# Kernel tuning notes

Hardware: AMD Instinct MI355X
Metric: run time of the kernel (lower is better)

## Reference

```python
import jax, jax.numpy as jnp
import numpy as np

N_NODES = 50000
N_EDGES = 1600000
IN_CH = 128
HEADS = 4
HEAD_DIM = 32  # out_channels // heads = 128 // 4
NEG_SLOPE = 0.2


def setup_inputs() -> dict:
    key = jax.random.key(0)
    ks = jax.random.split(key, 6)
    x = jax.random.normal(ks[0], (N_NODES, IN_CH), dtype=jnp.float32)
    edge_index = jax.random.randint(ks[1], (2, N_EDGES), 0, N_NODES, dtype=jnp.int64)
    W = jax.random.normal(ks[2], (IN_CH, HEADS * HEAD_DIM), dtype=jnp.float32) * 0.1
    att_src = jax.random.normal(ks[3], (HEADS, HEAD_DIM), dtype=jnp.float32) * 0.1
    att_dst = jax.random.normal(ks[4], (HEADS, HEAD_DIM), dtype=jnp.float32) * 0.1
    bias = jax.random.normal(ks[5], (HEADS * HEAD_DIM,), dtype=jnp.float32) * 0.1
    return {"x": x, "edge_index": edge_index, "W": W,
            "att_src": att_src, "att_dst": att_dst, "bias": bias}


def reference(x, edge_index, W, att_src, att_dst, bias):
    N = x.shape[0]
    # linear projection, split heads: [N, H, C]
    h = (x @ W).reshape(N, HEADS, HEAD_DIM)
    # per-node attention logits: [N, H]
    a_src = jnp.einsum('nhc,hc->nh', h, att_src)
    a_dst = jnp.einsum('nhc,hc->nh', h, att_dst)
    # add self loops (PyG default)
    loops = jnp.arange(N, dtype=edge_index.dtype)
    src = jnp.concatenate([edge_index[0], loops])  # message source j
    dst = jnp.concatenate([edge_index[1], loops])  # message target i
    # edge attention scores: [E_total, H]
    alpha = jax.nn.leaky_relu(a_src[src] + a_dst[dst], NEG_SLOPE)
    # segment softmax over incoming edges per destination node
    amax = jax.ops.segment_max(alpha, dst, num_segments=N)
    alpha = jnp.exp(alpha - amax[dst])
    denom = jax.ops.segment_sum(alpha, dst, num_segments=N)
    alpha = alpha / (denom[dst] + 1e-16)
    # weighted scatter-aggregate: [N, H, C]
    msg = h[src] * alpha[:, :, None]
    out = jax.ops.segment_sum(msg, dst, num_segments=N)
    out = out.reshape(N, HEADS * HEAD_DIM) + bias
    return jax.nn.elu(out)
```

## Files before the change

kernel.cpp:

```cpp
#include <hip/hip_runtime.h>

typedef unsigned short u16;
typedef unsigned int u32;

#define CH 128
#define NHEAD 4
#define NEG_SLOPE 0.2f
#define ROWS_PER_BLOCK 32
#define XPAD 132

#define LOG_NPB 7
#define NPB 128
#define NBMAX 400
#define BCAP 6144
#define KMB 6
#define GPAD 16
#define BINA_BLOCKS 256

typedef __attribute__((ext_vector_type(8))) short bf16x8;
typedef __attribute__((ext_vector_type(4))) float f32x4;

static __device__ __forceinline__ float bitf(u32 i) {
    float f; __builtin_memcpy(&f, &i, 4); return f;
}
static __device__ __forceinline__ float bflo(u32 v) { return bitf(v << 16); }
static __device__ __forceinline__ float bfhi(u32 v) { return bitf(v & 0xffff0000u); }
static __device__ __forceinline__ u16 f2bf(float f) {
    u32 i; __builtin_memcpy(&i, &f, 4);
    return (u16)((i + 0x7fffu + ((i >> 16) & 1u)) >> 16);
}
static __device__ __forceinline__ float lrelu(float v) { return v > 0.f ? v : NEG_SLOPE * v; }

static __device__ __forceinline__ int ei_at(const int* __restrict__ ei, int mode32, size_t idx) {
    return mode32 ? ei[idx] : ei[2 * idx];
}

__global__ __launch_bounds__(256) void init_kernel(
    const float* __restrict__ W, uint4* __restrict__ Wsw, int* __restrict__ gcur, int nGcur)
{
    const int t = blockIdx.x * 256 + threadIdx.x;
    if (t < 2048) {
        const int lane = t & 63, ks = (t >> 6) & 3, nt = t >> 8;
        const int col = nt * 16 + (lane & 15);
        const int kb = ks * 32 + ((lane >> 4) << 2);
        u16 v[8];
#pragma unroll
        for (int j = 0; j < 8; ++j) {
            int kk = kb + (j & 3) + ((j >> 2) << 4);
            v[j] = f2bf(W[(size_t)kk * CH + col]);
        }
        uint4 q;
        q.x = (u32)v[0] | ((u32)v[1] << 16);
        q.y = (u32)v[2] | ((u32)v[3] << 16);
        q.z = (u32)v[4] | ((u32)v[5] << 16);
        q.w = (u32)v[6] | ((u32)v[7] << 16);
        Wsw[t] = q;
    }
    for (int i = t; i < nGcur; i += 4096) gcur[i] = 0;
}

__global__ __launch_bounds__(256) void gemmbin_kernel(
    const float* __restrict__ x, const uint4* __restrict__ Wsw,
    const float* __restrict__ att_src, const float* __restrict__ att_dst,
    u16* __restrict__ h, float* __restrict__ asrc, float* __restrict__ adst, int N,
    const int* __restrict__ ei, int* __restrict__ gcur, u32* __restrict__ rec,
    int E, int NB)
{
    __shared__ float xs[ROWS_PER_BLOCK][XPAD];
    __shared__ uint4 Wb[2048];

    const int tid = threadIdx.x;

    if (blockIdx.x < BINA_BLOCKS) {
        int* hist  = (int*)&xs[0][0];
        int* hbase = hist + NBMAX;
        int* hcur  = hbase + NBMAX;
        const int mode32 = __syncthreads_or(ei[2 * tid + 1] != 0);
        for (int b = tid; b < NB; b += 256) { hist[b] = 0; hcur[b] = 0; }
        __syncthreads();
        const int chunk = (E + BINA_BLOCKS - 1) / BINA_BLOCKS;
        const int beg0 = blockIdx.x * chunk;
        const int end0 = min(E, beg0 + chunk);
#pragma unroll 4
        for (int e = beg0 + tid; e < end0; e += 256) {
            int dj = ei_at(ei, mode32, (size_t)E + e);
            atomicAdd(&hist[dj >> LOG_NPB], 1);
        }
        __syncthreads();
        for (int b = tid; b < NB; b += 256) {
            int c = hist[b];
            hbase[b] = c ? atomicAdd(&gcur[b * GPAD], c) : 0;
        }
        __syncthreads();
#pragma unroll 4
        for (int e = beg0 + tid; e < end0; e += 256) {
            int dj = ei_at(ei, mode32, (size_t)E + e);
            int sj = ei_at(ei, mode32, (size_t)e);
            int bkt = dj >> LOG_NPB;
            int r = atomicAdd(&hcur[bkt], 1);
            int pos = hbase[bkt] + r;
            if (pos < BCAP)
                rec[(size_t)bkt * BCAP + pos] = ((u32)sj << LOG_NPB) | (u32)(dj & (NPB - 1));
        }
        return;
    }

    const int gb = blockIdx.x - BINA_BLOCKS;
    const int r0b = gb * ROWS_PER_BLOCK;
#pragma unroll
    for (int i = 0; i < 8; ++i) Wb[tid + i * 256] = Wsw[tid + i * 256];
#pragma unroll
    for (int i = 0; i < 4; ++i) {
        int f = tid + i * 256;
        int row = f >> 5;
        int col = (f & 31) * 4;
        if (r0b + row < N)
            *(float4*)&xs[row][col] = *(const float4*)(x + (size_t)(r0b + row) * CH + col);
    }
    __syncthreads();

    const int lane = tid & 63;
    const int w = tid >> 6;
    const int g = lane >> 4;
    const int a15 = lane & 15;
    const int rt = w & 1;
    const int cb4 = w >> 1;

    f32x4 acc[4] = {};

#pragma unroll
    for (int ks = 0; ks < 4; ++ks) {
        const float* xr = &xs[rt * 16 + a15][ks * 32 + g * 4];
        float4 av0 = *(const float4*)xr;
        float4 av1 = *(const float4*)(xr + 16);
        float av[8] = {av0.x, av0.y, av0.z, av0.w, av1.x, av1.y, av1.z, av1.w};
        bf16x8 ahi, alo;
#pragma unroll
        for (int j = 0; j < 8; ++j) {
            u16 hb = f2bf(av[j]);
            ahi[j] = (short)hb;
            alo[j] = (short)f2bf(av[j] - bflo(hb));
        }
#pragma unroll
        for (int ct = 0; ct < 4; ++ct) {
            bf16x8 b = *(const bf16x8*)&Wb[((cb4 * 4 + ct) * 4 + ks) * 64 + lane];
            acc[ct] = __builtin_amdgcn_mfma_f32_16x16x32_bf16(alo, b, acc[ct], 0, 0, 0);
            acc[ct] = __builtin_amdgcn_mfma_f32_16x16x32_bf16(ahi, b, acc[ct], 0, 0, 0);
        }
    }

    float as_c[4], ad_c[4];
#pragma unroll
    for (int ct = 0; ct < 4; ++ct) {
        int c = cb4 * 64 + ct * 16 + a15;
        as_c[ct] = att_src[c];
        ad_c[ct] = att_dst[c];
    }
#pragma unroll
    for (int i = 0; i < 4; ++i) {
        float s0 = acc[0][i] * as_c[0] + acc[1][i] * as_c[1];
        float s1 = acc[2][i] * as_c[2] + acc[3][i] * as_c[3];
        float d0 = acc[0][i] * ad_c[0] + acc[1][i] * ad_c[1];
        float d1 = acc[2][i] * ad_c[2] + acc[3][i] * ad_c[3];
#pragma unroll
        for (int o = 1; o < 16; o <<= 1) {
            s0 += __shfl_xor(s0, o, 64);
            s1 += __shfl_xor(s1, o, 64);
            d0 += __shfl_xor(d0, o, 64);
            d1 += __shfl_xor(d1, o, 64);
        }
        if (a15 == 0) {
            int row = r0b + rt * 16 + g * 4 + i;
            if (row < N) {
                int hb0 = cb4 * 2;
                asrc[row * NHEAD + hb0]     = s0;
                asrc[row * NHEAD + hb0 + 1] = s1;
                adst[row * NHEAD + hb0]     = d0;
                adst[row * NHEAD + hb0 + 1] = d1;
            }
        }
    }

    __syncthreads();
    u16* ht = (u16*)&xs[0][0];
#pragma unroll
    for (int ct = 0; ct < 4; ++ct)
#pragma unroll
        for (int i = 0; i < 4; ++i)
            ht[(rt * 16 + g * 4 + i) * CH + cb4 * 64 + ct * 16 + a15] = f2bf(acc[ct][i]);
    __syncthreads();
    {
        const u32* ht32 = (const u32*)&xs[0][0];
        const int rw = w * 8;
#pragma unroll
        for (int r = 0; r < 8; ++r) {
            int row = r0b + rw + r;
            if (row < N)
                *(u32*)(h + (size_t)row * CH + lane * 2) = ht32[(rw + r) * 64 + lane];
        }
    }
}

__global__ __launch_bounds__(1024) void binBagg_kernel(
    const u16* __restrict__ h, const float* __restrict__ asrc, const float* __restrict__ adst,
    const int* __restrict__ gcur, const u32* __restrict__ rec,
    const float* __restrict__ bias, float* __restrict__ out, int N)
{
    __shared__ int outb[BCAP + 32];
    __shared__ int lcnt[NPB];
    __shared__ int lsc[NPB];
    __shared__ int lcur[NPB];
    const int tid = threadIdx.x;
    const int bkt = blockIdx.x;
    int cnt0 = gcur[bkt * GPAD];
    cnt0 = cnt0 < BCAP ? cnt0 : BCAP;
    const size_t rbase = (size_t)bkt * BCAP;

    if (tid < NPB) { lcnt[tid] = 0; lcur[tid] = 0; }

    u32 rc[KMB];
#pragma unroll
    for (int k = 0; k < KMB; ++k) {
        int i = tid + k * 1024;
        rc[k] = (i < cnt0) ? rec[rbase + i] : 0xffffffffu;
    }
    __syncthreads();
#pragma unroll
    for (int k = 0; k < KMB; ++k)
        if (rc[k] != 0xffffffffu) atomicAdd(&lcnt[rc[k] & (NPB - 1)], 1);
    __syncthreads();
    if (tid < NPB) lsc[tid] = lcnt[tid];
    __syncthreads();
    for (int o = 1; o < NPB; o <<= 1) {
        int v = (tid < NPB && tid >= o) ? lsc[tid - o] : 0;
        __syncthreads();
        if (tid < NPB) lsc[tid] += v;
        __syncthreads();
    }
#pragma unroll
    for (int k = 0; k < KMB; ++k) {
        if (rc[k] != 0xffffffffu) {
            int local = rc[k] & (NPB - 1);
            int r = atomicAdd(&lcur[local], 1);
            int slot = (lsc[local] - lcnt[local]) + r;
            outb[slot] = (int)(rc[k] >> LOG_NPB);
        }
    }
    __syncthreads();

    const int lane = tid & 63;
    const int wave = tid >> 6;
    const int g = lane >> 4;
    const int l = lane & 15;
    const int c8 = l * 8;
    const int head = l >> 2;

    for (int nl = 0; nl < 8; ++nl) {
        const int local = wave * 8 + nl;
        const int node = (bkt << LOG_NPB) + local;
        if (node >= N) continue;
        const int beg = lsc[local] - lcnt[local];
        const int end = lsc[local];
        const float4 ad4 = *(const float4*)(adst + node * 4);
        const float adh = (head == 0) ? ad4.x : (head == 1) ? ad4.y : (head == 2) ? ad4.z : ad4.w;
        const float4 asl = *(const float4*)(asrc + node * 4);
        const float aslh = (head == 0) ? asl.x : (head == 1) ? asl.y : (head == 2) ? asl.z : asl.w;
        const float mh = lrelu(aslh + adh);

        float acc[8];
#pragma unroll
        for (int k = 0; k < 8; ++k) acc[k] = 0.f;
        float s = 0.f;

        int e = beg + g;
        if (e < end) {
            uint4 hC[4]; float aC[4];
#pragma unroll
            for (int i = 0; i < 4; ++i) {
                int ei = e + 4 * i;
                int j = outb[ei];
                j = ((u32)j < (u32)N) ? j : 0;
                float a = asrc[j * NHEAD + head];
                aC[i] = (ei < end) ? a : -1e30f;
                hC[i] = *(const uint4*)(h + (size_t)j * CH + c8);
            }
            for (;;) {
                const int ebase = e + 16;
                uint4 hP[4]; float aP[4];
#pragma unroll
                for (int i = 0; i < 4; ++i) {
                    int ei = ebase + 4 * i;
                    int j = outb[ei];
                    j = ((u32)j < (u32)N) ? j : 0;
                    float a = asrc[j * NHEAD + head];
                    aP[i] = (ei < end) ? a : -1e30f;
                    hP[i] = *(const uint4*)(h + (size_t)j * CH + c8);
                }
#pragma unroll
                for (int i = 0; i < 4; ++i) {
                    float w = __expf(lrelu(aC[i] + adh) - mh);
                    s += w;
                    acc[0] = fmaf(w, bflo(hC[i].x), acc[0]);
                    acc[1] = fmaf(w, bfhi(hC[i].x), acc[1]);
                    acc[2] = fmaf(w, bflo(hC[i].y), acc[2]);
                    acc[3] = fmaf(w, bfhi(hC[i].y), acc[3]);
                    acc[4] = fmaf(w, bflo(hC[i].z), acc[4]);
                    acc[5] = fmaf(w, bfhi(hC[i].z), acc[5]);
                    acc[6] = fmaf(w, bflo(hC[i].w), acc[6]);
                    acc[7] = fmaf(w, bfhi(hC[i].w), acc[7]);
                }
#pragma unroll
                for (int i = 0; i < 4; ++i) { aC[i] = aP[i]; hC[i] = hP[i]; }
                e = ebase;
                if (e >= end) break;
            }
        }
        if (g == 0) {
            s += 1.0f;
            uint4 hv = *(const uint4*)(h + (size_t)node * CH + c8);
            acc[0] += bflo(hv.x);
            acc[1] += bfhi(hv.x);
            acc[2] += bflo(hv.y);
            acc[3] += bfhi(hv.y);
            acc[4] += bflo(hv.z);
            acc[5] += bfhi(hv.z);
            acc[6] += bflo(hv.w);
            acc[7] += bfhi(hv.w);
        }
#pragma unroll
        for (int o = 16; o < 64; o <<= 1) {
            s += __shfl_xor(s, o, 64);
#pragma unroll
            for (int k = 0; k < 8; ++k) acc[k] += __shfl_xor(acc[k], o, 64);
        }
        if (g == 0) {
            const float inv = 1.f / (s + 1e-16f);
            float o0[8];
#pragma unroll
            for (int k = 0; k < 8; ++k) {
                float v = acc[k] * inv + bias[c8 + k];
                o0[k] = v > 0.f ? v : __expf(v) - 1.f;
            }
            float4 lo = make_float4(o0[0], o0[1], o0[2], o0[3]);
            float4 hi = make_float4(o0[4], o0[5], o0[6], o0[7]);
            *(float4*)(out + (size_t)node * CH + c8) = lo;
            *(float4*)(out + (size_t)node * CH + c8 + 4) = hi;
        }
    }
}

extern "C" void kernel_launch(void* const* d_in, const int* in_sizes, int n_in,
                              void* d_out, int out_size, void* d_ws, size_t ws_size,
                              hipStream_t stream)
{
    const float* x       = (const float*)d_in[0];
    const int*   ei      = (const int*)d_in[1];
    const float* W       = (const float*)d_in[2];
    const float* att_src = (const float*)d_in[3];
    const float* att_dst = (const float*)d_in[4];
    const float* bias    = (const float*)d_in[5];
    float* out = (float*)d_out;
    const int N = in_sizes[0] / CH;
    const int E = in_sizes[1] / 2;
    const int NB = (N + NPB - 1) / NPB;

    char* p = (char*)d_ws;
    auto alloc = [&](size_t bytes) { char* r = p; p += (bytes + 255) & ~(size_t)255; return r; };
    u16*   h    = (u16*)alloc((size_t)N * CH * 2);
    float* asrc = (float*)alloc((size_t)N * NHEAD * 4);
    float* adst = (float*)alloc((size_t)N * NHEAD * 4);
    int*   gcur = (int*)alloc((size_t)NB * GPAD * 4);
    u32*   rec  = (u32*)alloc((size_t)NB * BCAP * 4);
    uint4* Wsw  = (uint4*)alloc((size_t)2048 * 16);

    const int gemmBlocks = (N + ROWS_PER_BLOCK - 1) / ROWS_PER_BLOCK;
    init_kernel<<<16, 256, 0, stream>>>(W, Wsw, gcur, NB * GPAD);
    gemmbin_kernel<<<BINA_BLOCKS + gemmBlocks, 256, 0, stream>>>(
        x, Wsw, att_src, att_dst, h, asrc, adst, N, ei, gcur, rec, E, NB);
    binBagg_kernel<<<NB, 1024, 0, stream>>>(h, asrc, adst, gcur, rec, bias, out, N);
}
```

Measured before the change: 197.3 us.

## Split fused bin-sort/aggregate kernel into CSR build and per-node aggregation kernels

The fused kernel that sorted bucketed edges in shared memory and then aggregated 128 nodes per 1024-thread block is split in two. A 256-thread sort kernel now writes a CSR array plus begin/degree arrays to global memory. A separate aggregation kernel handles one node per wave over N/4 blocks, which should improve load balance and occupancy. The cost is an extra launch and a global round trip for the CSR indices, about 6.4MB written and then read back.

```diff
diff --git a/kernel.cpp b/kernel.cpp
--- a/kernel.cpp
+++ b/kernel.cpp
@@ -13,7 +13,7 @@
 #define NPB 128
 #define NBMAX 400
 #define BCAP 6144
-#define KMB 6
+#define KMAX 24
 #define GPAD 16
 #define BINA_BLOCKS 256
 
@@ -201,12 +201,11 @@
     }
 }
 
-__global__ __launch_bounds__(1024) void binBagg_kernel(
-    const u16* __restrict__ h, const float* __restrict__ asrc, const float* __restrict__ adst,
+__global__ __launch_bounds__(256) void binB_kernel(
     const int* __restrict__ gcur, const u32* __restrict__ rec,
-    const float* __restrict__ bias, float* __restrict__ out, int N)
-{
-    __shared__ int outb[BCAP + 32];
+    int* __restrict__ csr, int* __restrict__ begA, int* __restrict__ degA, int N)
+{
+    __shared__ int outb[BCAP];
     __shared__ int lcnt[NPB];
     __shared__ int lsc[NPB];
     __shared__ int lcur[NPB];
@@ -218,15 +217,15 @@
 
     if (tid < NPB) { lcnt[tid] = 0; lcur[tid] = 0; }
 
-    u32 rc[KMB];
-#pragma unroll
-    for (int k = 0; k < KMB; ++k) {
-        int i = tid + k * 1024;
+    u32 rc[KMAX];
+#pragma unroll
+    for (int k = 0; k < KMAX; ++k) {
+        int i = tid + k * 256;
         rc[k] = (i < cnt0) ? rec[rbase + i] : 0xffffffffu;
     }
     __syncthreads();
 #pragma unroll
-    for (int k = 0; k < KMB; ++k)
+    for (int k = 0; k < KMAX; ++k)
         if (rc[k] != 0xffffffffu) atomicAdd(&lcnt[rc[k] & (NPB - 1)], 1);
     __syncthreads();
     if (tid < NPB) lsc[tid] = lcnt[tid];
@@ -238,7 +237,7 @@
         __syncthreads();
     }
 #pragma unroll
-    for (int k = 0; k < KMB; ++k) {
+    for (int k = 0; k < KMAX; ++k) {
         if (rc[k] != 0xffffffffu) {
             int local = rc[k] & (NPB - 1);
             int r = atomicAdd(&lcur[local], 1);
@@ -247,105 +246,116 @@
         }
     }
     __syncthreads();
-
-    const int lane = tid & 63;
-    const int wave = tid >> 6;
+    for (int i = tid; i < cnt0; i += 256)
+        csr[rbase + i] = outb[i];
+    if (tid < NPB) {
+        int node = (bkt << LOG_NPB) + tid;
+        if (node < N) {
+            begA[node] = (int)rbase + (lsc[tid] - lcnt[tid]);
+            degA[node] = lcnt[tid];
+        }
+    }
+}
+
+__global__ __launch_bounds__(256) void agg_kernel(
+    const u16* __restrict__ h, const float* __restrict__ asrc, const float* __restrict__ adst,
+    const int* __restrict__ begA, const int* __restrict__ degA, const int* __restrict__ csr,
+    const float* __restrict__ bias, float* __restrict__ out, int N)
+{
+    const int lane = threadIdx.x & 63;
+    const int wave = threadIdx.x >> 6;
+    const int node = blockIdx.x * 4 + wave;
+    if (node >= N) return;
     const int g = lane >> 4;
     const int l = lane & 15;
     const int c8 = l * 8;
     const int head = l >> 2;
-
-    for (int nl = 0; nl < 8; ++nl) {
-        const int local = wave * 8 + nl;
-        const int node = (bkt << LOG_NPB) + local;
-        if (node >= N) continue;
-        const int beg = lsc[local] - lcnt[local];
-        const int end = lsc[local];
-        const float4 ad4 = *(const float4*)(adst + node * 4);
-        const float adh = (head == 0) ? ad4.x : (head == 1) ? ad4.y : (head == 2) ? ad4.z : ad4.w;
-        const float4 asl = *(const float4*)(asrc + node * 4);
-        const float aslh = (head == 0) ? asl.x : (head == 1) ? asl.y : (head == 2) ? asl.z : asl.w;
-        const float mh = lrelu(aslh + adh);
-
-        float acc[8];
-#pragma unroll
-        for (int k = 0; k < 8; ++k) acc[k] = 0.f;
-        float s = 0.f;
-
-        int e = beg + g;
-        if (e < end) {
-            uint4 hC[4]; float aC[4];
+    const int beg = begA[node];
+    const int end = beg + degA[node];
+    const float4 ad4 = *(const float4*)(adst + node * 4);
+    const float adh = (head == 0) ? ad4.x : (head == 1) ? ad4.y : (head == 2) ? ad4.z : ad4.w;
+    const float4 asl = *(const float4*)(asrc + node * 4);
+    const float aslh = (head == 0) ? asl.x : (head == 1) ? asl.y : (head == 2) ? asl.z : asl.w;
+    const float mh = lrelu(aslh + adh);
+
+    float acc[8];
+#pragma unroll
+    for (int k = 0; k < 8; ++k) acc[k] = 0.f;
+    float s = 0.f;
+
+    int e = beg + g;
+    if (e < end) {
+        uint4 hC[4]; float aC[4];
+#pragma unroll
+        for (int i = 0; i < 4; ++i) {
+            int ei = e + 4 * i;
+            int j = csr[ei];
+            j = ((u32)j < (u32)N) ? j : 0;
+            float a = asrc[j * NHEAD + head];
+            aC[i] = (ei < end) ? a : -1e30f;
+            hC[i] = *(const uint4*)(h + (size_t)j * CH + c8);
+        }
+        for (;;) {
+            const int ebase = e + 16;
+            uint4 hP[4]; float aP[4];
 #pragma unroll
             for (int i = 0; i < 4; ++i) {
-                int ei = e + 4 * i;
-                int j = outb[ei];
+                int ei = ebase + 4 * i;
+                int j = csr[ei];
                 j = ((u32)j < (u32)N) ? j : 0;
                 float a = asrc[j * NHEAD + head];
-                aC[i] = (ei < end) ? a : -1e30f;
-                hC[i] = *(const uint4*)(h + (size_t)j * CH + c8);
+                aP[i] = (ei < end) ? a : -1e30f;
+                hP[i] = *(const uint4*)(h + (size_t)j * CH + c8);
             }
-            for (;;) {
-                const int ebase = e + 16;
-                uint4 hP[4]; float aP[4];
-#pragma unroll
-                for (int i = 0; i < 4; ++i) {
-                    int ei = ebase + 4 * i;
-                    int j = outb[ei];
-                    j = ((u32)j < (u32)N) ? j : 0;
-                    float a = asrc[j * NHEAD + head];
-                    aP[i] = (ei < end) ? a : -1e30f;
-                    hP[i] = *(const uint4*)(h + (size_t)j * CH + c8);
-                }
-#pragma unroll
-                for (int i = 0; i < 4; ++i) {
-                    float w = __expf(lrelu(aC[i] + adh) - mh);
-                    s += w;
-                    acc[0] = fmaf(w, bflo(hC[i].x), acc[0]);
-                    acc[1] = fmaf(w, bfhi(hC[i].x), acc[1]);
-                    acc[2] = fmaf(w, bflo(hC[i].y), acc[2]);
-                    acc[3] = fmaf(w, bfhi(hC[i].y), acc[3]);
-                    acc[4] = fmaf(w, bflo(hC[i].z), acc[4]);
-                    acc[5] = fmaf(w, bfhi(hC[i].z), acc[5]);
-                    acc[6] = fmaf(w, bflo(hC[i].w), acc[6]);
-                    acc[7] = fmaf(w, bfhi(hC[i].w), acc[7]);
-                }
-#pragma unroll
-                for (int i = 0; i < 4; ++i) { aC[i] = aP[i]; hC[i] = hP[i]; }
-                e = ebase;
-                if (e >= end) break;
+#pragma unroll
+            for (int i = 0; i < 4; ++i) {
+                float w = __expf(lrelu(aC[i] + adh) - mh);
+                s += w;
+                acc[0] = fmaf(w, bflo(hC[i].x), acc[0]);
+                acc[1] = fmaf(w, bfhi(hC[i].x), acc[1]);
+                acc[2] = fmaf(w, bflo(hC[i].y), acc[2]);
+                acc[3] = fmaf(w, bfhi(hC[i].y), acc[3]);
+                acc[4] = fmaf(w, bflo(hC[i].z), acc[4]);
+                acc[5] = fmaf(w, bfhi(hC[i].z), acc[5]);
+                acc[6] = fmaf(w, bflo(hC[i].w), acc[6]);
+                acc[7] = fmaf(w, bfhi(hC[i].w), acc[7]);
             }
-        }
-        if (g == 0) {
-            s += 1.0f;
-            uint4 hv = *(const uint4*)(h + (size_t)node * CH + c8);
-            acc[0] += bflo(hv.x);
-            acc[1] += bfhi(hv.x);
-            acc[2] += bflo(hv.y);
-            acc[3] += bfhi(hv.y);
-            acc[4] += bflo(hv.z);
-            acc[5] += bfhi(hv.z);
-            acc[6] += bflo(hv.w);
-            acc[7] += bfhi(hv.w);
-        }
-#pragma unroll
-        for (int o = 16; o < 64; o <<= 1) {
-            s += __shfl_xor(s, o, 64);
-#pragma unroll
-            for (int k = 0; k < 8; ++k) acc[k] += __shfl_xor(acc[k], o, 64);
-        }
-        if (g == 0) {
-            const float inv = 1.f / (s + 1e-16f);
-            float o0[8];
-#pragma unroll
-            for (int k = 0; k < 8; ++k) {
-                float v = acc[k] * inv + bias[c8 + k];
-                o0[k] = v > 0.f ? v : __expf(v) - 1.f;
-            }
-            float4 lo = make_float4(o0[0], o0[1], o0[2], o0[3]);
-            float4 hi = make_float4(o0[4], o0[5], o0[6], o0[7]);
-            *(float4*)(out + (size_t)node * CH + c8) = lo;
-            *(float4*)(out + (size_t)node * CH + c8 + 4) = hi;
-        }
+#pragma unroll
+            for (int i = 0; i < 4; ++i) { aC[i] = aP[i]; hC[i] = hP[i]; }
+            e = ebase;
+            if (e >= end) break;
+        }
+    }
+    if (g == 0) {
+        s += 1.0f;
+        uint4 hv = *(const uint4*)(h + (size_t)node * CH + c8);
+        acc[0] += bflo(hv.x);
+        acc[1] += bfhi(hv.x);
+        acc[2] += bflo(hv.y);
+        acc[3] += bfhi(hv.y);
+        acc[4] += bflo(hv.z);
+        acc[5] += bfhi(hv.z);
+        acc[6] += bflo(hv.w);
+        acc[7] += bfhi(hv.w);
+    }
+#pragma unroll
+    for (int o = 16; o < 64; o <<= 1) {
+        s += __shfl_xor(s, o, 64);
+#pragma unroll
+        for (int k = 0; k < 8; ++k) acc[k] += __shfl_xor(acc[k], o, 64);
+    }
+    if (g == 0) {
+        const float inv = 1.f / (s + 1e-16f);
+        float o0[8];
+#pragma unroll
+        for (int k = 0; k < 8; ++k) {
+            float v = acc[k] * inv + bias[c8 + k];
+            o0[k] = v > 0.f ? v : __expf(v) - 1.f;
+        }
+        float4 lo = make_float4(o0[0], o0[1], o0[2], o0[3]);
+        float4 hi = make_float4(o0[4], o0[5], o0[6], o0[7]);
+        *(float4*)(out + (size_t)node * CH + c8) = lo;
+        *(float4*)(out + (size_t)node * CH + c8 + 4) = hi;
     }
 }
 
@@ -371,11 +381,15 @@
     float* adst = (float*)alloc((size_t)N * NHEAD * 4);
     int*   gcur = (int*)alloc((size_t)NB * GPAD * 4);
     u32*   rec  = (u32*)alloc((size_t)NB * BCAP * 4);
+    int*   csr  = (int*)alloc((size_t)NB * BCAP * 4 + 256);
+    int*   begA = (int*)alloc((size_t)N * 4);
+    int*   degA = (int*)alloc((size_t)N * 4);
     uint4* Wsw  = (uint4*)alloc((size_t)2048 * 16);
 
     const int gemmBlocks = (N + ROWS_PER_BLOCK - 1) / ROWS_PER_BLOCK;
     init_kernel<<<16, 256, 0, stream>>>(W, Wsw, gcur, NB * GPAD);
     gemmbin_kernel<<<BINA_BLOCKS + gemmBlocks, 256, 0, stream>>>(
         x, Wsw, att_src, att_dst, h, asrc, adst, N, ei, gcur, rec, E, NB);
-    binBagg_kernel<<<NB, 1024, 0, stream>>>(h, asrc, adst, gcur, rec, bias, out, N);
-}
+    binB_kernel<<<NB, 256, 0, stream>>>(gcur, rec, csr, begA, degA, N);
+    agg_kernel<<<(N + 3) / 4, 256, 0, stream>>>(h, asrc, adst, begA, degA, csr, bias, out, N);
+}
```

New measurement: 191.0 us (median of 2 runs). 3.2% less time.
